# Performance work log

Hardware: AMD Instinct MI355X
Metric: run time of the kernel (lower is better)

Reference implementation:

```python
import jax, jax.numpy as jnp
import numpy as np

B, S, D, H = 2, 2048, 2048, 16
HD = D // H


def setup_inputs() -> dict:
    key = jax.random.key(0)
    kx, = jax.random.split(key, 1)
    return {
        "x": jax.random.normal(kx, (B, S, D), dtype=jnp.float32),
        "q_mask": jnp.ones((D, D), dtype=jnp.float32),
        "k_mask": jnp.ones((D, D), dtype=jnp.float32),
        "v_mask": jnp.ones((D, D), dtype=jnp.float32),
        "out_mask": jnp.ones((D, D), dtype=jnp.float32),
        "head_mask": jnp.ones((H,), dtype=jnp.float32),
        "attention_mask": jnp.ones((B, S), dtype=jnp.float32),
        "shared_weight": jnp.float32(1.0),
    }


def reference(x, q_mask, k_mask, v_mask, out_mask, head_mask, attention_mask, shared_weight):
    b, s, d = x.shape
    scale = jnp.float32(HD) ** -0.5

    def shared_linear(inp, mask):
        # F.linear(x, mask * shared_weight): out = inp @ (mask*sw).T
        return jnp.einsum("bsd,ed->bse", inp, mask * shared_weight)

    q = shared_linear(x, q_mask).reshape(b, s, H, HD).transpose(0, 2, 1, 3)  # [B,H,S,HD]
    k = shared_linear(x, k_mask).reshape(b, s, H, HD).transpose(0, 2, 1, 3)
    v = shared_linear(x, v_mask).reshape(b, s, H, HD).transpose(0, 2, 1, 3)

    hm = head_mask.reshape(1, H, 1, 1)
    q, k, v = q * hm, k * hm, v * hm

    scores = jnp.einsum("bhqd,bhkd->bhqk", q, k) * scale  # [B,H,S,S]

    # causal mask: upper triangle (j > i) -> -inf
    causal = jnp.triu(jnp.ones((s, s), dtype=bool), k=1)
    scores = jnp.where(causal, -jnp.inf, scores)

    # additive attention mask: (1 - m) * -10000, broadcast [B,1,1,S]
    scores = scores + (1.0 - attention_mask)[:, None, None, :] * -10000.0

    attn = jax.nn.softmax(scores, axis=-1)  # dropout is identity in eval / p=0

    out = jnp.einsum("bhqk,bhkd->bhqd", attn, v)          # [B,H,S,HD]
    out = out.transpose(0, 2, 1, 3).reshape(b, s, d)       # [B,S,D]
    return shared_linear(out, out_mask)
```

## Files before the change

### kernel.cpp

```cpp
#include <hip/hip_runtime.h>

#define B_  2
#define S_  2048
#define D_  2048
#define H_  16
#define HD_ 128

typedef __bf16 bf16;
typedef __bf16 bf16x4 __attribute__((ext_vector_type(4)));
typedef __bf16 bf16x8 __attribute__((ext_vector_type(8)));
typedef float  f32x4  __attribute__((ext_vector_type(4)));
typedef unsigned int u32x4 __attribute__((ext_vector_type(4)));

__device__ __forceinline__ void gld_lds16(const void* g, void* l) {
    __builtin_amdgcn_global_load_lds(
        (const __attribute__((address_space(1))) unsigned int*)g,
        (__attribute__((address_space(3))) unsigned int*)l, 16, 0, 0);
}

__device__ __forceinline__ f32x4 mfma16(bf16x8 a, bf16x8 b, f32x4 c) {
    return __builtin_amdgcn_mfma_f32_16x16x32_bf16(a, b, c, 0, 0, 0);
}

#define BAR()  asm volatile("s_barrier" ::: "memory")
#define SBAR() __builtin_amdgcn_sched_barrier(0)

__global__ __launch_bounds__(256)
void precast_all(const float* __restrict__ x, bf16* __restrict__ xh,
                 bf16* __restrict__ xl,
                 const float* __restrict__ qm, bf16* __restrict__ qmb,
                 const float* __restrict__ km, bf16* __restrict__ kmb,
                 const float* __restrict__ swp) {
    int bid = blockIdx.x;
    if (bid < 4096) {
        int i = (bid * 256 + threadIdx.x) * 8;
        float4 a = *(const float4*)(x + i);
        float4 b = *(const float4*)(x + i + 4);
        float av[8] = {a.x, a.y, a.z, a.w, b.x, b.y, b.z, b.w};
        bf16x8 h8, l8;
#pragma unroll
        for (int e = 0; e < 8; e++) {
            bf16 hv = (bf16)av[e];
            h8[e] = hv;
            l8[e] = (bf16)(av[e] - (float)hv);
        }
        *(bf16x8*)(xh + i) = h8;
        *(bf16x8*)(xl + i) = l8;
        return;
    }
    const float sw = swp[0];
    bid -= 4096;
    const float* src = qm; bf16* dst = qmb;
    if (bid >= 2048) { src = km; dst = kmb; bid -= 2048; }
    int i = (bid * 256 + threadIdx.x) * 8;
    float4 a = *(const float4*)(src + i);
    float4 b = *(const float4*)(src + i + 4);
    bf16x8 o;
    o[0] = (bf16)(a.x * sw); o[1] = (bf16)(a.y * sw);
    o[2] = (bf16)(a.z * sw); o[3] = (bf16)(a.w * sw);
    o[4] = (bf16)(b.x * sw); o[5] = (bf16)(b.y * sw);
    o[6] = (bf16)(b.z * sw); o[7] = (bf16)(b.w * sw);
    *(bf16x8*)(dst + i) = o;
}

__global__ __launch_bounds__(256)
void precast_mask(const float* __restrict__ s0, bf16* __restrict__ d0,
                  const float* __restrict__ swp) {
    const float sw = swp[0];
    int i = (blockIdx.x * 256 + threadIdx.x) * 8;
    float4 a = *(const float4*)(s0 + i);
    float4 b = *(const float4*)(s0 + i + 4);
    bf16x8 o;
    o[0] = (bf16)(a.x * sw); o[1] = (bf16)(a.y * sw);
    o[2] = (bf16)(a.z * sw); o[3] = (bf16)(a.w * sw);
    o[4] = (bf16)(b.x * sw); o[5] = (bf16)(b.y * sw);
    o[6] = (bf16)(b.z * sw); o[7] = (bf16)(b.w * sw);
    *(bf16x8*)(d0 + i) = o;
}

template<int BM, int BN, int MODE>
__global__ __launch_bounds__(256, 2)
void gemm2p(const bf16* __restrict__ Ah_g, const bf16* __restrict__ Al_g,
            const bf16* __restrict__ Bq, const bf16* __restrict__ Bk,
            const float* __restrict__ hm,
            bf16* __restrict__ o_qh, bf16* __restrict__ o_ql,
            bf16* __restrict__ o_kh, bf16* __restrict__ o_kl,
            bf16* __restrict__ o_vt, float* __restrict__ o_f32,
            int nt) {
    constexpr int IM = BM / 2 / 16;
    constexpr int JN = BN / 2 / 16;
    constexpr int IH = IM / 2;
    constexpr int ISSA = BM / 64;
    constexpr int ISSB = BN / 64;
    constexpr int BUFE = (BM + BN) * 32;
    constexpr int SMELEMS = (MODE == 1 && BN * (BM + 8) > 2 * BUFE)
                                ? BN * (BM + 8) : 2 * BUFE;
    __shared__ bf16 sm[SMELEMS];

    const int t = threadIdx.x;
    const int wave = t >> 6, lane = t & 63;
    const int lrow = lane & 15, quad = lane >> 4;
    const int wr = wave >> 1, wc = wave & 1;

    const int gx = gridDim.x;
    const int id0 = blockIdx.y * gx + blockIdx.x;
    const int nwg = gx * gridDim.y;
    const int id = (id0 & 7) * (nwg >> 3) + (id0 >> 3);
    const int m0 = (id / gx) * BM, n0 = (id % gx) * BN;

    const int nsec = (MODE == 0) ? (n0 & (D_ - 1)) : n0;
    const bf16* Bg = (MODE == 0 && n0 >= D_) ? Bk : Bq;

    const int arow = wr * (BM / 2) + lrow;
    const int brow = wc * (BN / 2) + lrow;
    const int gsw = (quad ^ ((lrow >> 1) & 3)) * 8;

    const int srr = lane >> 2, spg = lane & 3;
    const int ssw = (spg ^ ((srr >> 1) & 3)) * 8;

    auto stage_A = [&](int kt, int pbuf) {
        const bf16* As = (MODE == 0 && kt >= 64) ? Al_g : Ah_g;
        const int kc = ((MODE == 0) ? (kt & 63) : kt) * 32;
        bf16* buf = sm + pbuf * BUFE;
#pragma unroll
        for (int pp = 0; pp < ISSA; pp++) {
            int r0 = wave * (BM / 4) + pp * 16;
            gld_lds16(As + (size_t)(m0 + r0 + srr) * D_ + kc + ssw,
                      buf + r0 * 32);
        }
    };
    auto stage_B = [&](int kt, int pbuf) {
        const int kc = ((MODE == 0) ? (kt & 63) : kt) * 32;
        bf16* buf = sm + pbuf * BUFE + BM * 32;
#pragma unroll
        for (int pp = 0; pp < ISSB; pp++) {
            int r0 = wave * (BN / 4) + pp * 16;
            gld_lds16(Bg + (size_t)(nsec + r0 + srr) * D_ + kc + ssw,
                      buf + r0 * 32);
        }
    };

    f32x4 acc[IM][JN];
#pragma unroll
    for (int i = 0; i < IM; i++)
#pragma unroll
        for (int j = 0; j < JN; j++) acc[i][j] = (f32x4){0.f, 0.f, 0.f, 0.f};

    stage_A(0, 0); stage_B(0, 0); stage_B(1, 1);

    int p = 0;
    for (int kt = 0; kt < nt; ++kt) {
        if (kt < nt - 1) asm volatile("s_waitcnt vmcnt(2)" ::: "memory");
        else             asm volatile("s_waitcnt vmcnt(0)" ::: "memory");
        BAR();
        if (kt + 1 < nt) stage_A(kt + 1, p ^ 1);

        const bf16* Ab = sm + p * BUFE;
        const bf16* Bb = Ab + BM * 32;
        bf16x8 b[JN], au[IH], al[IH];

#pragma unroll
        for (int j = 0; j < JN; j++)
            b[j] = *(const bf16x8*)&Bb[(brow + j * 16) * 32 + gsw];
#pragma unroll
        for (int i = 0; i < IH; i++)
            au[i] = *(const bf16x8*)&Ab[(arow + i * 16) * 32 + gsw];
        SBAR();
#pragma unroll
        for (int i = 0; i < IH; i++)
            al[i] = *(const bf16x8*)&Ab[(arow + (IH + i) * 16) * 32 + gsw];
        SBAR();
        if constexpr (IH == 4) asm volatile("s_waitcnt lgkmcnt(4)" ::: "memory");
        else                   asm volatile("s_waitcnt lgkmcnt(2)" ::: "memory");
        SBAR();
        __builtin_amdgcn_s_setprio(1);
#pragma unroll
        for (int i = 0; i < IH; i++)
#pragma unroll
            for (int j = 0; j < JN; j++)
                acc[i][j] = mfma16(au[i], b[j], acc[i][j]);
        __builtin_amdgcn_s_setprio(0);
        BAR();

        if (kt + 2 < nt) stage_B(kt + 2, p);

        asm volatile("s_waitcnt lgkmcnt(0)" ::: "memory");
        SBAR();
        __builtin_amdgcn_s_setprio(1);
#pragma unroll
        for (int i = 0; i < IH; i++)
#pragma unroll
            for (int j = 0; j < JN; j++)
                acc[IH + i][j] = mfma16(al[i], b[j], acc[IH + i][j]);
        __builtin_amdgcn_s_setprio(0);
        p ^= 1;
    }

    if constexpr (MODE == 0) {
        const bool isq = (n0 < D_);
        bf16* oh = isq ? o_qh : o_kh;
        bf16* ol = isq ? o_ql : o_kl;
#pragma unroll
        for (int j = 0; j < JN; j++) {
            int nb = nsec + wc * (BN / 2) + j * 16;
            int h = nb >> 7;
            float hv = hm[h];
#pragma unroll
            for (int i = 0; i < IM; i++) {
                int mB = m0 + wr * (BM / 2) + i * 16 + quad * 4;
                int bb = mB >> 11, s = mB & (S_ - 1);
                size_t idx0 = (((size_t)bb * H_ + h) * S_ + s) * HD_ + (nb & 127) + lrow;
#pragma unroll
                for (int r = 0; r < 4; r++) {
                    float v = acc[i][j][r] * hv;
                    bf16 hvv = (bf16)v;
                    bf16 lvv = (bf16)(v - (float)hvv);
                    oh[idx0 + (size_t)r * HD_] = hvv;
                    ol[idx0 + (size_t)r * HD_] = lvv;
                }
            }
        }
    }
    if constexpr (MODE == 1) {
        __syncthreads();
        bf16* tr = sm;
#pragma unroll
        for (int j = 0; j < JN; j++) {
            int nl = wc * (BN / 2) + j * 16 + lrow;
            float hv = hm[(n0 + nl) >> 7];
#pragma unroll
            for (int i = 0; i < IM; i++) {
                int ml = wr * (BM / 2) + i * 16 + quad * 4;
                bf16x4 pk;
#pragma unroll
                for (int r = 0; r < 4; r++) pk[r] = (bf16)(acc[i][j][r] * hv);
                *(bf16x4*)&tr[nl * 136 + ml] = pk;
            }
        }
        __syncthreads();
        const int bI = m0 >> 11;
        const int s0 = m0 & (S_ - 1);
#pragma unroll
        for (int w = 0; w < 8; w++) {
            int nrow = w * 16 + (t >> 4);
            int c = t & 15;
            bf16x8 vv = *(const bf16x8*)&tr[nrow * 136 + c * 8];
            int ng = n0 + nrow;
            int h = ng >> 7, hd = ng & 127;
            *(bf16x8*)&o_vt[((size_t)(bI * H_ + h) * HD_ + hd) * S_ + s0 + c * 8] = vv;
        }
    }
    if constexpr (MODE == 2) {
#pragma unroll
        for (int j = 0; j < JN; j++) {
            int n = n0 + wc * (BN / 2) + j * 16 + lrow;
#pragma unroll
            for (int i = 0; i < IM; i++) {
                int mB = m0 + wr * (BM / 2) + i * 16 + quad * 4;
#pragma unroll
                for (int r = 0; r < 4; r++)
                    o_f32[(size_t)(mB + r) * D_ + n] = acc[i][j][r];
            }
        }
    }
}

#define SPLD 72

__global__ __launch_bounds__(256, 2)
void attn_kernel(const bf16* __restrict__ qh_, const bf16* __restrict__ ql_,
                 const bf16* __restrict__ kh_, const bf16* __restrict__ kl_,
                 const bf16* __restrict__ vt_, const float* __restrict__ am,
                 bf16* __restrict__ outp) {
    const int bh = blockIdx.x & 31;
    const int qblk = 31 - (blockIdx.x >> 5);
    const int b = bh >> 4, h = bh & 15;
    const int i0 = qblk * 64;
    const int t = threadIdx.x, wave = t >> 6, lane = t & 63;
    const int lrow = lane & 15, quad = lane >> 4;

    __shared__ bf16 skh[64 * 128];
    __shared__ bf16 skl[64 * 128];
    __shared__ bf16 svt[128 * 64];
    __shared__ bf16 sp[4][16 * SPLD];

    const size_t kbase = (size_t)bh * S_ * HD_;
    const size_t vbase = (size_t)bh * HD_ * S_;

    const int qrow = i0 + wave * 16 + lrow;
    bf16x8 qhf[4], qlf[4];
#pragma unroll
    for (int c = 0; c < 4; c++) {
        qhf[c] = *(const bf16x8*)&qh_[kbase + (size_t)qrow * HD_ + c * 32 + quad * 8];
        qlf[c] = *(const bf16x8*)&ql_[kbase + (size_t)qrow * HD_ + c * 32 + quad * 8];
    }

    u32x4 kpre[8], vpre[4];
    auto issueKV = [&](int j0) {
#pragma unroll
        for (int p = 0; p < 4; p++) {
            int rb = wave * 16 + p * 4;
            int r = rb + (lane >> 4);
            int gl = ((lane & 15) ^ (r & 7)) * 8;
            kpre[p]     = *(const u32x4*)(kh_ + kbase + (size_t)(j0 + r) * HD_ + gl);
            kpre[4 + p] = *(const u32x4*)(kl_ + kbase + (size_t)(j0 + r) * HD_ + gl);
        }
#pragma unroll
        for (int p = 0; p < 4; p++) {
            int db = wave * 32 + p * 8;
            int d = db + (lane >> 3);
            int gl = ((lane & 7) ^ (d & 7)) * 8;
            vpre[p] = *(const u32x4*)(vt_ + vbase + (size_t)d * S_ + j0 + gl);
        }
    };
    auto writeKV = [&]() {
#pragma unroll
        for (int p = 0; p < 4; p++) {
            int rb = wave * 16 + p * 4;
            *(u32x4*)&skh[rb * 128 + lane * 8] = kpre[p];
            *(u32x4*)&skl[rb * 128 + lane * 8] = kpre[4 + p];
        }
#pragma unroll
        for (int p = 0; p < 4; p++) {
            int db = wave * 32 + p * 8;
            *(u32x4*)&svt[db * 64 + lane * 8] = vpre[p];
        }
    };

    float m_i[4], l_i[4];
    f32x4 O[8];
#pragma unroll
    for (int r = 0; r < 4; r++) { m_i[r] = -INFINITY; l_i[r] = 0.f; }
#pragma unroll
    for (int n2 = 0; n2 < 8; n2++) O[n2] = (f32x4){0.f, 0.f, 0.f, 0.f};

    const float scale = 0.08838834764831845f;

    issueKV(0);

    for (int j0 = 0; j0 <= i0; j0 += 64) {
        asm volatile("s_waitcnt vmcnt(0)" ::: "memory");
        BAR();
        writeKV();
        if (j0 + 64 <= i0) issueKV(j0 + 64);
        asm volatile("s_waitcnt lgkmcnt(0)" ::: "memory");
        BAR();

        float amadd[4];
#pragma unroll
        for (int nt = 0; nt < 4; nt++)
            amadd[nt] = (1.0f - am[b * S_ + j0 + nt * 16 + lrow]) * -10000.0f;

        f32x4 s4[4];
#pragma unroll
        for (int nt = 0; nt < 4; nt++) s4[nt] = (f32x4){0.f, 0.f, 0.f, 0.f};
        __builtin_amdgcn_s_setprio(1);
#pragma unroll
        for (int c = 0; c < 4; c++) {
#pragma unroll
            for (int nt = 0; nt < 4; nt++) {
                int ka = (nt * 16 + lrow) * 128 + (((c * 4 + quad) ^ (lrow & 7)) * 8);
                bf16x8 kb8 = *(const bf16x8*)&skh[ka];
                bf16x8 lb8 = *(const bf16x8*)&skl[ka];
                s4[nt] = mfma16(qhf[c], kb8, s4[nt]);
                s4[nt] = mfma16(qhf[c], lb8, s4[nt]);
                s4[nt] = mfma16(qlf[c], kb8, s4[nt]);
            }
        }
        __builtin_amdgcn_s_setprio(0);

        const bool diag = (j0 == i0);
#pragma unroll
        for (int r = 0; r < 4; r++) {
            const int rrow = wave * 16 + quad * 4 + r;
            float sv[4], pw[4];
            float mx = -INFINITY;
#pragma unroll
            for (int nt = 0; nt < 4; nt++) {
                float xv = s4[nt][r] * scale + amadd[nt];
                if (diag && (nt * 16 + lrow) > rrow) xv = -INFINITY;
                sv[nt] = xv;
                mx = fmaxf(mx, xv);
            }
#pragma unroll
            for (int off = 1; off < 16; off <<= 1) mx = fmaxf(mx, __shfl_xor(mx, off));
            float mnew = fmaxf(m_i[r], mx);
            float alpha = __expf(m_i[r] - mnew);
            float ps = 0.f;
#pragma unroll
            for (int nt = 0; nt < 4; nt++) { pw[nt] = __expf(sv[nt] - mnew); ps += pw[nt]; }
#pragma unroll
            for (int off = 1; off < 16; off <<= 1) ps += __shfl_xor(ps, off);
            l_i[r] = l_i[r] * alpha + ps;
            m_i[r] = mnew;
#pragma unroll
            for (int n2 = 0; n2 < 8; n2++) O[n2][r] *= alpha;
#pragma unroll
            for (int nt = 0; nt < 4; nt++)
                sp[wave][(quad * 4 + r) * SPLD + nt * 16 + lrow] = (bf16)pw[nt];
        }
        asm volatile("s_waitcnt lgkmcnt(0)" ::: "memory");

        __builtin_amdgcn_s_setprio(1);
#pragma unroll
        for (int k2 = 0; k2 < 2; k2++) {
            bf16x8 pf = *(const bf16x8*)&sp[wave][lrow * SPLD + k2 * 32 + quad * 8];
            const int gp = ((quad + k2 * 4) ^ (lrow & 7)) * 8;
#pragma unroll
            for (int n2 = 0; n2 < 8; n2++) {
                bf16x8 vf8 = *(const bf16x8*)&svt[(n2 * 16 + lrow) * 64 + gp];
                O[n2] = mfma16(pf, vf8, O[n2]);
            }
        }
        __builtin_amdgcn_s_setprio(0);
    }

    float inv[4];
#pragma unroll
    for (int r = 0; r < 4; r++) inv[r] = 1.0f / l_i[r];
#pragma unroll
    for (int n2 = 0; n2 < 8; n2++)
#pragma unroll
        for (int r = 0; r < 4; r++) {
            int srow = i0 + wave * 16 + quad * 4 + r;
            outp[((size_t)(b * S_ + srow)) * D_ + h * HD_ + n2 * 16 + lrow] =
                (bf16)(O[n2][r] * inv[r]);
        }
}

extern "C" void kernel_launch(void* const* d_in, const int* in_sizes, int n_in,
                              void* d_out, int out_size, void* d_ws, size_t ws_size,
                              hipStream_t stream) {
    const float* x  = (const float*)d_in[0];
    const float* qm = (const float*)d_in[1];
    const float* km = (const float*)d_in[2];
    const float* vm = (const float*)d_in[3];
    const float* om = (const float*)d_in[4];
    const float* hm = (const float*)d_in[5];
    const float* am = (const float*)d_in[6];
    const float* sw = (const float*)d_in[7];
    float* out = (float*)d_out;

    const size_t P = (size_t)B_ * H_ * S_ * HD_ * sizeof(bf16);
    char* ws = (char*)d_ws;
    bf16* xh = (bf16*)(ws + 0 * P);
    bf16* xl = (bf16*)(ws + 1 * P);
    bf16* qh = (bf16*)(ws + 2 * P);
    bf16* ql = (bf16*)(ws + 3 * P);
    bf16* kh = (bf16*)(ws + 4 * P);
    bf16* kl = (bf16*)(ws + 5 * P);
    bf16* attn_out = xh;
    bf16* vmb = xl;
    bf16* omb = qh;
    bf16* vt  = (bf16*)d_out;
    bf16* qmb = (bf16*)((char*)d_out + 16u * 1024 * 1024);
    bf16* kmb = (bf16*)((char*)d_out + 24u * 1024 * 1024);

    precast_all<<<8192, 256, 0, stream>>>(x, xh, xl, qm, qmb, km, kmb, sw);

    gemm2p<256, 128, 0><<<dim3(32, 16), 256, 0, stream>>>(
        xh, xl, qmb, kmb, hm, qh, ql, kh, kl, nullptr, nullptr, 128);

    precast_mask<<<2048, 256, 0, stream>>>(vm, vmb, sw);
    gemm2p<128, 128, 1><<<dim3(16, 32), 256, 0, stream>>>(
        xh, nullptr, vmb, nullptr, hm,
        nullptr, nullptr, nullptr, nullptr, vt, nullptr, 64);

    attn_kernel<<<1024, 256, 0, stream>>>(qh, ql, kh, kl, vt, am, attn_out);

    precast_mask<<<2048, 256, 0, stream>>>(om, omb, sw);
    gemm2p<128, 128, 2><<<dim3(16, 32), 256, 0, stream>>>(
        attn_out, nullptr, omb, nullptr, hm,
        nullptr, nullptr, nullptr, nullptr, nullptr, out, 64);
}
```

Baseline: 490.6 us.

## Remap attention blocks per XCD, cache mask in LDS, reorder GEMM LDS loads

The attention grid is remapped so that all query blocks of one batch-head land on the same XCD, which is meant to improve L2 reuse of K/V. The additive attention mask is precomputed once per block into shared memory instead of being reloaded from global memory on every KV tile. The explicit vmcnt wait is dropped and replaced by a syncthreads before the loop. In the projection GEMM, the second half of the A fragments is now loaded after the first MFMA batch, reusing the same registers. This adds an extra barrier and a full LDS wait, trading register pressure against overlap of loads with compute.

```diff
diff --git a/kernel.cpp b/kernel.cpp
--- a/kernel.cpp
+++ b/kernel.cpp
@@ -23,7 +23,8 @@
 }
 
 #define BAR()  asm volatile("s_barrier" ::: "memory")
-#define SBAR() __builtin_amdgcn_sched_barrier(0)
+#define WAIT_LGKM0() do { asm volatile("s_waitcnt lgkmcnt(0)" ::: "memory"); \
+                          __builtin_amdgcn_sched_barrier(0); } while (0)
 
 __global__ __launch_bounds__(256)
 void precast_all(const float* __restrict__ x, bf16* __restrict__ xh,
@@ -157,41 +158,37 @@
 
         const bf16* Ab = sm + p * BUFE;
         const bf16* Bb = Ab + BM * 32;
-        bf16x8 b[JN], au[IH], al[IH];
+        bf16x8 a[IH], b[JN];
 
 #pragma unroll
         for (int j = 0; j < JN; j++)
             b[j] = *(const bf16x8*)&Bb[(brow + j * 16) * 32 + gsw];
 #pragma unroll
         for (int i = 0; i < IH; i++)
-            au[i] = *(const bf16x8*)&Ab[(arow + i * 16) * 32 + gsw];
-        SBAR();
+            a[i] = *(const bf16x8*)&Ab[(arow + i * 16) * 32 + gsw];
+        BAR();
+        WAIT_LGKM0();
+        __builtin_amdgcn_s_setprio(1);
 #pragma unroll
         for (int i = 0; i < IH; i++)
-            al[i] = *(const bf16x8*)&Ab[(arow + (IH + i) * 16) * 32 + gsw];
-        SBAR();
-        if constexpr (IH == 4) asm volatile("s_waitcnt lgkmcnt(4)" ::: "memory");
-        else                   asm volatile("s_waitcnt lgkmcnt(2)" ::: "memory");
-        SBAR();
-        __builtin_amdgcn_s_setprio(1);
-#pragma unroll
-        for (int i = 0; i < IH; i++)
 #pragma unroll
             for (int j = 0; j < JN; j++)
-                acc[i][j] = mfma16(au[i], b[j], acc[i][j]);
+                acc[i][j] = mfma16(a[i], b[j], acc[i][j]);
         __builtin_amdgcn_s_setprio(0);
         BAR();
 
         if (kt + 2 < nt) stage_B(kt + 2, p);
 
-        asm volatile("s_waitcnt lgkmcnt(0)" ::: "memory");
-        SBAR();
+#pragma unroll
+        for (int i = 0; i < IH; i++)
+            a[i] = *(const bf16x8*)&Ab[(arow + (IH + i) * 16) * 32 + gsw];
+        WAIT_LGKM0();
         __builtin_amdgcn_s_setprio(1);
 #pragma unroll
         for (int i = 0; i < IH; i++)
 #pragma unroll
             for (int j = 0; j < JN; j++)
-                acc[IH + i][j] = mfma16(al[i], b[j], acc[IH + i][j]);
+                acc[IH + i][j] = mfma16(a[i], b[j], acc[IH + i][j]);
         __builtin_amdgcn_s_setprio(0);
         p ^= 1;
     }
@@ -272,8 +269,10 @@
                  const bf16* __restrict__ kh_, const bf16* __restrict__ kl_,
                  const bf16* __restrict__ vt_, const float* __restrict__ am,
                  bf16* __restrict__ outp) {
-    const int bh = blockIdx.x & 31;
-    const int qblk = 31 - (blockIdx.x >> 5);
+    const int id = blockIdx.x;
+    const int xcd = id & 7, slot = id >> 3;
+    const int bh = xcd * 4 + (slot & 3);
+    const int qblk = 31 - (slot >> 2);
     const int b = bh >> 4, h = bh & 15;
     const int i0 = qblk * 64;
     const int t = threadIdx.x, wave = t >> 6, lane = t & 63;
@@ -283,9 +282,22 @@
     __shared__ bf16 skl[64 * 128];
     __shared__ bf16 svt[128 * 64];
     __shared__ bf16 sp[4][16 * SPLD];
+    __shared__ float samadd[S_];
 
     const size_t kbase = (size_t)bh * S_ * HD_;
     const size_t vbase = (size_t)bh * HD_ * S_;
+
+    {
+        int j = t * 8;
+        float4 a0 = *(const float4*)(am + b * S_ + j);
+        float4 a1 = *(const float4*)(am + b * S_ + j + 4);
+        float4 r0 = {(1.0f - a0.x) * -10000.0f, (1.0f - a0.y) * -10000.0f,
+                     (1.0f - a0.z) * -10000.0f, (1.0f - a0.w) * -10000.0f};
+        float4 r1 = {(1.0f - a1.x) * -10000.0f, (1.0f - a1.y) * -10000.0f,
+                     (1.0f - a1.z) * -10000.0f, (1.0f - a1.w) * -10000.0f};
+        *(float4*)&samadd[j] = r0;
+        *(float4*)&samadd[j + 4] = r1;
+    }
 
     const int qrow = i0 + wave * 16 + lrow;
     bf16x8 qhf[4], qlf[4];
@@ -337,9 +349,9 @@
     const float scale = 0.08838834764831845f;
 
     issueKV(0);
+    __syncthreads();
 
     for (int j0 = 0; j0 <= i0; j0 += 64) {
-        asm volatile("s_waitcnt vmcnt(0)" ::: "memory");
         BAR();
         writeKV();
         if (j0 + 64 <= i0) issueKV(j0 + 64);
@@ -349,7 +361,7 @@
         float amadd[4];
 #pragma unroll
         for (int nt = 0; nt < 4; nt++)
-            amadd[nt] = (1.0f - am[b * S_ + j0 + nt * 16 + lrow]) * -10000.0f;
+            amadd[nt] = samadd[j0 + nt * 16 + lrow];
 
         f32x4 s4[4];
 #pragma unroll
```

Result: no change. 488.4 us (-0.4%).
